# Performance work log

Hardware: AMD Instinct MI355X
Metric: run time of the kernel (lower is better)

The kernel has to match this reference:

```python
import jax, jax.numpy as jnp
import numpy as np

N_NODES = 100000
N_EDGES = 1600000
D_IN = 128
D_HID = 128
D_OUT = 128


def sage_conv(x, src, dst, W_l, b_l, W_r, n_nodes):
    # PyG SAGEConv (mean aggr): out = Linear_l(mean_j x_j) + Linear_r(x_i)
    msg = x[src]                                            # [E, d] gather
    agg = jax.ops.segment_sum(msg, dst, num_segments=n_nodes)  # [N, d]
    cnt = jax.ops.segment_sum(jnp.ones((src.shape[0],), x.dtype), dst,
                              num_segments=n_nodes)
    mean = agg / jnp.maximum(cnt, 1.0)[:, None]             # mean over neighbors
    return mean @ W_l.T + b_l + x @ W_r.T


def setup_inputs() -> dict:
    key = jax.random.key(0)
    ks = jax.random.split(key, 8)
    x = jax.random.normal(ks[0], (N_NODES, D_IN), dtype=jnp.float32)
    edge_index = jax.random.randint(ks[1], (2, N_EDGES), 0, N_NODES, dtype=jnp.int64)
    s1 = 1.0 / np.sqrt(D_IN)
    s2 = 1.0 / np.sqrt(D_HID)
    W1_l = jax.random.uniform(ks[2], (D_HID, D_IN), jnp.float32, -s1, s1)
    b1_l = jax.random.uniform(ks[3], (D_HID,), jnp.float32, -s1, s1)
    W1_r = jax.random.uniform(ks[4], (D_HID, D_IN), jnp.float32, -s1, s1)
    W2_l = jax.random.uniform(ks[5], (D_OUT, D_HID), jnp.float32, -s2, s2)
    b2_l = jax.random.uniform(ks[6], (D_OUT,), jnp.float32, -s2, s2)
    W2_r = jax.random.uniform(ks[7], (D_OUT, D_HID), jnp.float32, -s2, s2)
    return {"x": x, "edge_index": edge_index, "W1_l": W1_l, "b1_l": b1_l,
            "W1_r": W1_r, "W2_l": W2_l, "b2_l": b2_l, "W2_r": W2_r}


def reference(x, edge_index, W1_l, b1_l, W1_r, W2_l, b2_l, W2_r):
    src, dst = edge_index[0], edge_index[1]
    n = x.shape[0]
    h = sage_conv(x, src, dst, W1_l, b1_l, W1_r, n)
    h = jax.nn.relu(h)
    # F.dropout with training=False (eval mode) is identity
    out = sage_conv(h, src, dst, W2_l, b2_l, W2_r, n)
    return out
```

## Files before the change

### kernel.cpp

```cpp
#include <hip/hip_runtime.h>

typedef __attribute__((ext_vector_type(8))) short short8;
typedef __attribute__((ext_vector_type(4))) float f32x4;

#define NBMAX 512
#define CAP 8192

__device__ inline unsigned short f2bf(float f) {
  union { float f; unsigned u; } v; v.f = f;
  unsigned r = v.u + 0x7fffu + ((v.u >> 16) & 1u);
  return (unsigned short)(r >> 16);
}
__device__ inline float bf2f(unsigned short b) {
  union { unsigned u; float f; } v; v.u = ((unsigned)b) << 16;
  return v.f;
}

__device__ inline void addv8(float (&a)[8], uint4 v) {
  a[0] += bf2f((unsigned short)(v.x & 0xffffu));
  a[1] += bf2f((unsigned short)(v.x >> 16));
  a[2] += bf2f((unsigned short)(v.y & 0xffffu));
  a[3] += bf2f((unsigned short)(v.y >> 16));
  a[4] += bf2f((unsigned short)(v.z & 0xffffu));
  a[5] += bf2f((unsigned short)(v.z >> 16));
  a[6] += bf2f((unsigned short)(v.w & 0xffffu));
  a[7] += bf2f((unsigned short)(v.w >> 16));
}

__device__ inline int load_src(const int* ei, int E, int e, int f64) {
  return f64 ? ei[2 * e] : ei[e];
}
__device__ inline int load_dst(const int* ei, int E, int e, int f64) {
  return f64 ? ei[2 * (E + e)] : ei[E + e];
}

__global__ __launch_bounds__(256) void castbf(
    const float* __restrict__ x, unsigned short* __restrict__ xb, int n8,
    const float* __restrict__ W1l, const float* __restrict__ W1r,
    const float* __restrict__ W2l, const float* __restrict__ W2r,
    unsigned short* __restrict__ Wp) {
  const int nxb = gridDim.x - 4;
  const int b = blockIdx.x;
  const int tid = threadIdx.x;
  if (b >= nxb) {
    const int m = b - nxb;
    const float* W = (m == 0) ? W1l : (m == 1) ? W1r : (m == 2) ? W2l : W2r;
    unsigned short* dst = Wp + (size_t)m * 16384;
#pragma unroll
    for (int it = 0; it < 8; ++it) {
      int id = it * 256 + tid;
      int j = id >> 4;
      int kc = id & 15;
      int s = kc >> 2, q = kc & 3;
      int jt = j >> 4, nn2 = j & 15;
      int c = (s * 8 + jt) * 4 + q;
      const float* src = W + j * 128 + kc * 8;
      union { unsigned short u[8]; uint4 v; } t;
#pragma unroll
      for (int k = 0; k < 8; ++k) t.u[k] = f2bf(src[k]);
      *(uint4*)(dst + (c * 16 + nn2) * 8) = t.v;
    }
    return;
  }
  int i = b * 256 + tid;
  const int stride = nxb * 256;
  for (; i < n8; i += stride) {
    float4 v0 = ((const float4*)x)[2 * i];
    float4 v1 = ((const float4*)x)[2 * i + 1];
    union { unsigned short u[8]; uint4 v; } t;
    t.u[0] = f2bf(v0.x); t.u[1] = f2bf(v0.y);
    t.u[2] = f2bf(v0.z); t.u[3] = f2bf(v0.w);
    t.u[4] = f2bf(v1.x); t.u[5] = f2bf(v1.y);
    t.u[6] = f2bf(v1.z); t.u[7] = f2bf(v1.w);
    ((uint4*)xb)[i] = t.v;
  }
}

__global__ __launch_bounds__(256) void scatter2(
    const int* __restrict__ ei, int E,
    int* __restrict__ btot, int2* __restrict__ stage) {
  __shared__ int lcnt[NBMAX];
  __shared__ int lbase[NBMAX];
  __shared__ int sflag;
  const int t = threadIdx.x;
  if (t == 0) sflag = 0;
  for (int i = t; i < NBMAX; i += 256) lcnt[i] = 0;
  __syncthreads();
  const int e0 = blockIdx.x * 4096;
  {
    int e = e0 + t;
    int v = (e < E) ? ei[2 * e + 1] : 0;
    if (v) atomicOr(&sflag, 1);
  }
  __syncthreads();
  const int f64 = (sflag == 0) ? 1 : 0;

  int srcs[16], bks[16];
  int dsts[16];
#pragma unroll
  for (int i = 0; i < 16; ++i) {
    int e = e0 + i * 256 + t;
    if (e < E) {
      srcs[i] = load_src(ei, E, e, f64);
      int d = load_dst(ei, E, e, f64);
      dsts[i] = d;
      bks[i] = d >> 8;
      atomicAdd(&lcnt[d >> 8], 1);
    } else {
      bks[i] = -1;
    }
  }
  __syncthreads();
  for (int i = t; i < NBMAX; i += 256) {
    int c = lcnt[i];
    lbase[i] = c ? atomicAdd(&btot[i], c) : 0;
  }
  __syncthreads();
  for (int i = t; i < NBMAX; i += 256) lcnt[i] = 0;
  __syncthreads();
#pragma unroll
  for (int i = 0; i < 16; ++i) {
    int b = bks[i];
    if (b >= 0) {
      int r = atomicAdd(&lcnt[b], 1);
      stage[(size_t)b * CAP + lbase[b] + r] = make_int2(srcs[i], dsts[i]);
    }
  }
}

__global__ __launch_bounds__(256) void bucket_fill2(
    const int2* __restrict__ stage, const int* __restrict__ btot,
    int* __restrict__ offs, int* __restrict__ cnt, float* __restrict__ inv,
    int* __restrict__ csr, int N) {
  __shared__ int lhist[256];
  __shared__ int lscan[256];
  __shared__ int lcur[256];
  __shared__ int red[256];
  const int b = blockIdx.x;
  const int t = threadIdx.x;
  int sum = 0;
  for (int j = t; j < b; j += 256) sum += btot[j];
  red[t] = sum;
  lhist[t] = 0;
  __syncthreads();
  for (int d = 128; d; d >>= 1) {
    if (t < d) red[t] += red[t + d];
    __syncthreads();
  }
  const int base = red[0];
  const int count = btot[b];
  const int2* sp = stage + (size_t)b * CAP;
  for (int i = t; i < count; i += 256)
    atomicAdd(&lhist[sp[i].y & 255], 1);
  __syncthreads();
  int v = lhist[t];
  lscan[t] = v;
  __syncthreads();
  for (int d = 1; d < 256; d <<= 1) {
    int tv = (t >= d) ? lscan[t - d] : 0;
    __syncthreads();
    lscan[t] += tv;
    __syncthreads();
  }
  const int excl = lscan[t] - v;
  const int node = b * 256 + t;
  if (node < N) {
    offs[node] = base + excl;
    cnt[node] = v;
    inv[node] = 1.0f / (float)((v > 1) ? v : 1);
  }
  lcur[t] = base + excl;
  __syncthreads();
  for (int i = t; i < count; i += 256) {
    int2 sd = sp[i];
    int p = atomicAdd(&lcur[sd.y & 255], 1);
    csr[p] = sd.x;
  }
}

__global__ __launch_bounds__(256, 4) void agg_mean(
    const unsigned short* __restrict__ A, const float* __restrict__ inv,
    const int* __restrict__ offs, const int* __restrict__ cnt,
    const int* __restrict__ csr, unsigned short* __restrict__ M, int n) {
  int pr = (int)((blockIdx.x * 256 + threadIdx.x) >> 6);
  int n0 = pr * 2;
  if (n0 >= n) return;
  const int n1 = n0 + 1;
  const bool has1 = (n1 < n);
  const int lane = threadIdx.x & 63;
  const int g = lane >> 4;
  const int l = lane & 15;
  const int deg0 = cnt[n0];
  const int deg1 = has1 ? cnt[n1] : 0;
  const int start = offs[n0];
  const int T = deg0 + deg1;
  float acc0[8] = {0.f, 0.f, 0.f, 0.f, 0.f, 0.f, 0.f, 0.f};
  float acc1[8] = {0.f, 0.f, 0.f, 0.f, 0.f, 0.f, 0.f, 0.f};

  if (T <= 64) {
    int idx = (lane < T) ? csr[start + lane] : 0;
    int jmax = (T + 3) >> 2;
#pragma unroll 8
    for (int j = 0; j < jmax; ++j) {
      int e = j * 4 + g;
      int nbv = __shfl(idx, e);
      if (e < T) {
        uint4 v = *(const uint4*)(A + (size_t)nbv * 128 + l * 8);
        if (e < deg0) addv8(acc0, v);
        else addv8(acc1, v);
      }
    }
  } else {
    for (int node = 0; node < 2; ++node) {
      int dg = node ? deg1 : deg0;
      int st = node ? (start + deg0) : start;
      for (int base = 0; base < dg; base += 64) {
        int m = dg - base;
        if (m > 64) m = 64;
        int idx = (lane < m) ? csr[st + base + lane] : 0;
#pragma unroll 4
        for (int i = 0; i < m; i += 4) {
          int sl = i + g;
          int nbv = __shfl(idx, sl & 63);
          if (sl < m) {
            uint4 v = *(const uint4*)(A + (size_t)nbv * 128 + l * 8);
            if (node) addv8(acc1, v);
            else addv8(acc0, v);
          }
        }
      }
    }
  }

#pragma unroll
  for (int j = 0; j < 8; ++j) {
    acc0[j] += __shfl_xor(acc0[j], 16);
    acc0[j] += __shfl_xor(acc0[j], 32);
    acc1[j] += __shfl_xor(acc1[j], 16);
    acc1[j] += __shfl_xor(acc1[j], 32);
  }

  const int c0 = l * 8 + g * 2;
  {
    float s = inv[n0];
    unsigned pkt = (unsigned)f2bf(acc0[g * 2 + 0] * s) |
                   ((unsigned)f2bf(acc0[g * 2 + 1] * s) << 16);
    *(unsigned*)(M + (size_t)n0 * 128 + c0) = pkt;
  }
  if (has1) {
    float s = inv[n1];
    unsigned pkt = (unsigned)f2bf(acc1[g * 2 + 0] * s) |
                   ((unsigned)f2bf(acc1[g * 2 + 1] * s) << 16);
    *(unsigned*)(M + (size_t)n1 * 128 + c0) = pkt;
  }
}

template <int RELU, int OUTBF>
__global__ __launch_bounds__(256) void gemm_fused(
    const unsigned short* __restrict__ Am,
    const unsigned short* __restrict__ As,
    const unsigned short* __restrict__ Wp,
    const float* __restrict__ bias, void* __restrict__ outp, int n) {
  __shared__ unsigned short wsh[2 * 16384];
  const int tid = threadIdx.x;

  {
    const uint4* wsrc = (const uint4*)Wp;
    uint4* wdst = (uint4*)wsh;
#pragma unroll
    for (int it = 0; it < 16; ++it) {
      int id = it * 256 + tid;
      wdst[id] = wsrc[id];
    }
  }
  __syncthreads();

  const int lane = tid & 63;
  const int wave = tid >> 6;
  const int nn = lane & 15;
  const int quad = lane >> 4;
  const int rowbase = blockIdx.x * 64 + wave * 16;

  int nodeA = rowbase + nn;
  if (nodeA > n - 1) nodeA = n - 1;

  short8 am[4], asf[4];
#pragma unroll
  for (int s = 0; s < 4; ++s) {
    am[s] = *(const short8*)(Am + (size_t)nodeA * 128 + s * 32 + quad * 8);
    asf[s] = *(const short8*)(As + (size_t)nodeA * 128 + s * 32 + quad * 8);
  }

  f32x4 acc[8];
#pragma unroll
  for (int jt = 0; jt < 8; ++jt) acc[jt] = (f32x4){0.f, 0.f, 0.f, 0.f};

#pragma unroll
  for (int jt = 0; jt < 8; ++jt) {
#pragma unroll
    for (int s = 0; s < 4; ++s) {
      int c = (s * 8 + jt) * 4 + quad;
      short8 bl = *(const short8*)(wsh + (c * 16 + nn) * 8);
      short8 br = *(const short8*)(wsh + 16384 + (c * 16 + nn) * 8);
      acc[jt] = __builtin_amdgcn_mfma_f32_16x16x32_bf16(am[s], bl, acc[jt], 0, 0, 0);
      acc[jt] = __builtin_amdgcn_mfma_f32_16x16x32_bf16(asf[s], br, acc[jt], 0, 0, 0);
    }
  }

#pragma unroll
  for (int jt = 0; jt < 8; ++jt) {
    int col = jt * 16 + nn;
    float bv = bias[col];
#pragma unroll
    for (int r = 0; r < 4; ++r) {
      int ro = rowbase + quad * 4 + r;
      if (ro < n) {
        float o = acc[jt][r] + bv;
        if (RELU) o = fmaxf(o, 0.f);
        if (OUTBF) {
          ((unsigned short*)outp)[(size_t)ro * 128 + col] = f2bf(o);
        } else {
          ((float*)outp)[(size_t)ro * 128 + col] = o;
        }
      }
    }
  }
}


extern "C" void kernel_launch(void* const* d_in, const int* in_sizes, int n_in,
                              void* d_out, int out_size, void* d_ws, size_t ws_size,
                              hipStream_t stream) {
  const float* x = (const float*)d_in[0];
  const int* ei = (const int*)d_in[1];
  const float* W1l = (const float*)d_in[2];
  const float* b1 = (const float*)d_in[3];
  const float* W1r = (const float*)d_in[4];
  const float* W2l = (const float*)d_in[5];
  const float* b2 = (const float*)d_in[6];
  const float* W2r = (const float*)d_in[7];
  float* out = (float*)d_out;

  const int N = in_sizes[0] / 128;
  const int E = in_sizes[1] / 2;
  const int nb = (N + 255) / 256;

  char* p = (char*)d_ws;
  auto alloc = [&](size_t bytes) {
    char* r = p;
    p += (bytes + 255) & ~(size_t)255;
    return r;
  };
  int* btot = (int*)alloc((size_t)NBMAX * 4);
  int* cnt = (int*)alloc((size_t)N * 4);
  int* offs = (int*)alloc((size_t)N * 4);
  float* inv = (float*)alloc((size_t)N * 4);
  int* csr = (int*)alloc((size_t)E * 4);
  unsigned short* Mb = (unsigned short*)alloc((size_t)N * 128 * 2);
  unsigned short* Wpb = (unsigned short*)alloc((size_t)4 * 16384 * 2);
  size_t stage_bytes = (size_t)nb * CAP * 8;
  size_t hb_bytes = (size_t)N * 128 * 2;
  char* shared_region = alloc(stage_bytes > hb_bytes ? stage_bytes : hb_bytes);
  unsigned short* hb = (unsigned short*)shared_region;
  int2* stage = (int2*)shared_region;

  unsigned short* xb = (unsigned short*)d_out;

  hipMemsetAsync(btot, 0, (size_t)nb * 4, stream);

  castbf<<<2052, 256, 0, stream>>>(x, xb, N * 128 / 8, W1l, W1r, W2l, W2r, Wpb);
  scatter2<<<(E + 4095) / 4096, 256, 0, stream>>>(ei, E, btot, stage);
  bucket_fill2<<<nb, 256, 0, stream>>>(stage, btot, offs, cnt, inv, csr, N);

  const int gb = (N + 63) / 64;
  const int pairs = (N + 1) / 2;
  const int ab2 = (pairs + 3) / 4;

  agg_mean<<<ab2, 256, 0, stream>>>(xb, inv, offs, cnt, csr, Mb, N);
  gemm_fused<1, 1><<<gb, 256, 0, stream>>>(Mb, xb, Wpb, b1, (void*)hb, N);
  agg_mean<<<ab2, 256, 0, stream>>>(hb, inv, offs, cnt, csr, Mb, N);
  gemm_fused<0, 0><<<gb, 256, 0, stream>>>(Mb, hb, Wpb + 32768, b2, (void*)out, N);
}
```

Before: 344.3 us.

## Merge edge scatter with bf16 casts and batch neighbor loads in aggregation

Folds the edge-bucketing scatter kernel into the cast kernel so the x/weight conversions and scatter share one launch, with blocks split by index range. In agg_mean, the small-degree path now issues eight gathered row loads at once before accumulating, which raises memory-level parallelism. It also precomputes byte offsets (index<<8) and accumulates bf16 pairs into float2 vectors to cut unpack ALU work. This adds register pressure and loads padded lanes unconditionally (index 0 rows) when the degree is small.

```diff
diff --git a/kernel.cpp b/kernel.cpp
--- a/kernel.cpp
+++ b/kernel.cpp
@@ -2,6 +2,7 @@
 
 typedef __attribute__((ext_vector_type(8))) short short8;
 typedef __attribute__((ext_vector_type(4))) float f32x4;
+typedef __attribute__((ext_vector_type(2))) float f32x2;
 
 #define NBMAX 512
 #define CAP 8192
@@ -11,20 +12,13 @@
   unsigned r = v.u + 0x7fffu + ((v.u >> 16) & 1u);
   return (unsigned short)(r >> 16);
 }
-__device__ inline float bf2f(unsigned short b) {
-  union { unsigned u; float f; } v; v.u = ((unsigned)b) << 16;
-  return v.f;
-}
-
-__device__ inline void addv8(float (&a)[8], uint4 v) {
-  a[0] += bf2f((unsigned short)(v.x & 0xffffu));
-  a[1] += bf2f((unsigned short)(v.x >> 16));
-  a[2] += bf2f((unsigned short)(v.y & 0xffffu));
-  a[3] += bf2f((unsigned short)(v.y >> 16));
-  a[4] += bf2f((unsigned short)(v.z & 0xffffu));
-  a[5] += bf2f((unsigned short)(v.z >> 16));
-  a[6] += bf2f((unsigned short)(v.w & 0xffffu));
-  a[7] += bf2f((unsigned short)(v.w >> 16));
+
+__device__ inline void addf2(f32x2 (&a)[4], uint4 v) {
+  union { uint2 u; f32x2 f; } t;
+  t.u.x = v.x << 16; t.u.y = v.x & 0xffff0000u; a[0] += t.f;
+  t.u.x = v.y << 16; t.u.y = v.y & 0xffff0000u; a[1] += t.f;
+  t.u.x = v.z << 16; t.u.y = v.z & 0xffff0000u; a[2] += t.f;
+  t.u.x = v.w << 16; t.u.y = v.w & 0xffff0000u; a[3] += t.f;
 }
 
 __device__ inline int load_src(const int* ei, int E, int e, int f64) {
@@ -34,97 +28,100 @@
   return f64 ? ei[2 * (E + e)] : ei[E + e];
 }
 
-__global__ __launch_bounds__(256) void castbf(
+__global__ __launch_bounds__(256) void prep(
+    const int* __restrict__ ei, int E,
+    int* __restrict__ btot, int2* __restrict__ stage, int SB,
     const float* __restrict__ x, unsigned short* __restrict__ xb, int n8,
     const float* __restrict__ W1l, const float* __restrict__ W1r,
     const float* __restrict__ W2l, const float* __restrict__ W2r,
     unsigned short* __restrict__ Wp) {
-  const int nxb = gridDim.x - 4;
+  __shared__ int lcnt[NBMAX];
+  __shared__ int lbase[NBMAX];
+  __shared__ int sflag;
   const int b = blockIdx.x;
-  const int tid = threadIdx.x;
-  if (b >= nxb) {
-    const int m = b - nxb;
+  const int t = threadIdx.x;
+
+  if (b < SB) {
+    if (t == 0) sflag = 0;
+    for (int i = t; i < NBMAX; i += 256) lcnt[i] = 0;
+    __syncthreads();
+    const int e0 = b * 4096;
+    {
+      int e = e0 + t;
+      int v = (e < E) ? ei[2 * e + 1] : 0;
+      if (v) atomicOr(&sflag, 1);
+    }
+    __syncthreads();
+    const int f64 = (sflag == 0) ? 1 : 0;
+
+    int srcs[16], bks[16];
+    int dsts[16];
+#pragma unroll
+    for (int i = 0; i < 16; ++i) {
+      int e = e0 + i * 256 + t;
+      if (e < E) {
+        srcs[i] = load_src(ei, E, e, f64);
+        int d = load_dst(ei, E, e, f64);
+        dsts[i] = d;
+        bks[i] = d >> 8;
+        atomicAdd(&lcnt[d >> 8], 1);
+      } else {
+        bks[i] = -1;
+      }
+    }
+    __syncthreads();
+    for (int i = t; i < NBMAX; i += 256) {
+      int c = lcnt[i];
+      lbase[i] = c ? atomicAdd(&btot[i], c) : 0;
+    }
+    __syncthreads();
+    for (int i = t; i < NBMAX; i += 256) lcnt[i] = 0;
+    __syncthreads();
+#pragma unroll
+    for (int i = 0; i < 16; ++i) {
+      int bk = bks[i];
+      if (bk >= 0) {
+        int r = atomicAdd(&lcnt[bk], 1);
+        stage[(size_t)bk * CAP + lbase[bk] + r] = make_int2(srcs[i], dsts[i]);
+      }
+    }
+    return;
+  }
+
+  if (b < SB + 4) {
+    const int m = b - SB;
     const float* W = (m == 0) ? W1l : (m == 1) ? W1r : (m == 2) ? W2l : W2r;
     unsigned short* dst = Wp + (size_t)m * 16384;
 #pragma unroll
     for (int it = 0; it < 8; ++it) {
-      int id = it * 256 + tid;
+      int id = it * 256 + t;
       int j = id >> 4;
       int kc = id & 15;
       int s = kc >> 2, q = kc & 3;
       int jt = j >> 4, nn2 = j & 15;
       int c = (s * 8 + jt) * 4 + q;
       const float* src = W + j * 128 + kc * 8;
-      union { unsigned short u[8]; uint4 v; } t;
-#pragma unroll
-      for (int k = 0; k < 8; ++k) t.u[k] = f2bf(src[k]);
-      *(uint4*)(dst + (c * 16 + nn2) * 8) = t.v;
+      union { unsigned short u[8]; uint4 v; } tv;
+#pragma unroll
+      for (int k = 0; k < 8; ++k) tv.u[k] = f2bf(src[k]);
+      *(uint4*)(dst + (c * 16 + nn2) * 8) = tv.v;
     }
     return;
   }
-  int i = b * 256 + tid;
+
+  const int cb = b - SB - 4;
+  const int nxb = gridDim.x - SB - 4;
+  int i = cb * 256 + t;
   const int stride = nxb * 256;
   for (; i < n8; i += stride) {
     float4 v0 = ((const float4*)x)[2 * i];
     float4 v1 = ((const float4*)x)[2 * i + 1];
-    union { unsigned short u[8]; uint4 v; } t;
-    t.u[0] = f2bf(v0.x); t.u[1] = f2bf(v0.y);
-    t.u[2] = f2bf(v0.z); t.u[3] = f2bf(v0.w);
-    t.u[4] = f2bf(v1.x); t.u[5] = f2bf(v1.y);
-    t.u[6] = f2bf(v1.z); t.u[7] = f2bf(v1.w);
-    ((uint4*)xb)[i] = t.v;
-  }
-}
-
-__global__ __launch_bounds__(256) void scatter2(
-    const int* __restrict__ ei, int E,
-    int* __restrict__ btot, int2* __restrict__ stage) {
-  __shared__ int lcnt[NBMAX];
-  __shared__ int lbase[NBMAX];
-  __shared__ int sflag;
-  const int t = threadIdx.x;
-  if (t == 0) sflag = 0;
-  for (int i = t; i < NBMAX; i += 256) lcnt[i] = 0;
-  __syncthreads();
-  const int e0 = blockIdx.x * 4096;
-  {
-    int e = e0 + t;
-    int v = (e < E) ? ei[2 * e + 1] : 0;
-    if (v) atomicOr(&sflag, 1);
-  }
-  __syncthreads();
-  const int f64 = (sflag == 0) ? 1 : 0;
-
-  int srcs[16], bks[16];
-  int dsts[16];
-#pragma unroll
-  for (int i = 0; i < 16; ++i) {
-    int e = e0 + i * 256 + t;
-    if (e < E) {
-      srcs[i] = load_src(ei, E, e, f64);
-      int d = load_dst(ei, E, e, f64);
-      dsts[i] = d;
-      bks[i] = d >> 8;
-      atomicAdd(&lcnt[d >> 8], 1);
-    } else {
-      bks[i] = -1;
-    }
-  }
-  __syncthreads();
-  for (int i = t; i < NBMAX; i += 256) {
-    int c = lcnt[i];
-    lbase[i] = c ? atomicAdd(&btot[i], c) : 0;
-  }
-  __syncthreads();
-  for (int i = t; i < NBMAX; i += 256) lcnt[i] = 0;
-  __syncthreads();
-#pragma unroll
-  for (int i = 0; i < 16; ++i) {
-    int b = bks[i];
-    if (b >= 0) {
-      int r = atomicAdd(&lcnt[b], 1);
-      stage[(size_t)b * CAP + lbase[b] + r] = make_int2(srcs[i], dsts[i]);
-    }
+    union { unsigned short u[8]; uint4 v; } tv;
+    tv.u[0] = f2bf(v0.x); tv.u[1] = f2bf(v0.y);
+    tv.u[2] = f2bf(v0.z); tv.u[3] = f2bf(v0.w);
+    tv.u[4] = f2bf(v1.x); tv.u[5] = f2bf(v1.y);
+    tv.u[6] = f2bf(v1.z); tv.u[7] = f2bf(v1.w);
+    ((uint4*)xb)[i] = tv.v;
   }
 }
 
@@ -194,20 +191,40 @@
   const int deg1 = has1 ? cnt[n1] : 0;
   const int start = offs[n0];
   const int T = deg0 + deg1;
-  float acc0[8] = {0.f, 0.f, 0.f, 0.f, 0.f, 0.f, 0.f, 0.f};
-  float acc1[8] = {0.f, 0.f, 0.f, 0.f, 0.f, 0.f, 0.f, 0.f};
+  f32x2 acc0[4] = {{0.f, 0.f}, {0.f, 0.f}, {0.f, 0.f}, {0.f, 0.f}};
+  f32x2 acc1[4] = {{0.f, 0.f}, {0.f, 0.f}, {0.f, 0.f}, {0.f, 0.f}};
+  const char* Ab = (const char*)A + (size_t)l * 16;
 
   if (T <= 64) {
-    int idx = (lane < T) ? csr[start + lane] : 0;
-    int jmax = (T + 3) >> 2;
-#pragma unroll 8
-    for (int j = 0; j < jmax; ++j) {
-      int e = j * 4 + g;
-      int nbv = __shfl(idx, e);
-      if (e < T) {
-        uint4 v = *(const uint4*)(A + (size_t)nbv * 128 + l * 8);
-        if (e < deg0) addv8(acc0, v);
-        else addv8(acc1, v);
+    int offb = ((lane < T) ? csr[start + lane] : 0) << 8;
+    {
+      int nb[8];
+      uint4 vv[8];
+#pragma unroll
+      for (int j = 0; j < 8; ++j) nb[j] = __shfl(offb, j * 4 + g);
+#pragma unroll
+      for (int j = 0; j < 8; ++j)
+        vv[j] = *(const uint4*)(Ab + (size_t)(unsigned)nb[j]);
+#pragma unroll
+      for (int j = 0; j < 8; ++j) {
+        int e = j * 4 + g;
+        if (e < deg0) addf2(acc0, vv[j]);
+        else if (e < T) addf2(acc1, vv[j]);
+      }
+    }
+    if (T > 32) {
+      int nb[8];
+      uint4 vv[8];
+#pragma unroll
+      for (int j = 0; j < 8; ++j) nb[j] = __shfl(offb, 32 + j * 4 + g);
+#pragma unroll
+      for (int j = 0; j < 8; ++j)
+        vv[j] = *(const uint4*)(Ab + (size_t)(unsigned)nb[j]);
+#pragma unroll
+      for (int j = 0; j < 8; ++j) {
+        int e = 32 + j * 4 + g;
+        if (e < deg0) addf2(acc0, vv[j]);
+        else if (e < T) addf2(acc1, vv[j]);
       }
     }
   } else {
@@ -217,15 +234,15 @@
       for (int base = 0; base < dg; base += 64) {
         int m = dg - base;
         if (m > 64) m = 64;
-        int idx = (lane < m) ? csr[st + base + lane] : 0;
+        int offb = ((lane < m) ? csr[st + base + lane] : 0) << 8;
 #pragma unroll 4
         for (int i = 0; i < m; i += 4) {
           int sl = i + g;
-          int nbv = __shfl(idx, sl & 63);
+          int nbv = __shfl(offb, sl & 63);
           if (sl < m) {
-            uint4 v = *(const uint4*)(A + (size_t)nbv * 128 + l * 8);
-            if (node) addv8(acc1, v);
-            else addv8(acc0, v);
+            uint4 v = *(const uint4*)(Ab + (size_t)(unsigned)nbv);
+            if (node) addf2(acc1, v);
+            else addf2(acc0, v);
           }
         }
       }
@@ -233,24 +250,28 @@
   }
 
 #pragma unroll
-  for (int j = 0; j < 8; ++j) {
-    acc0[j] += __shfl_xor(acc0[j], 16);
-    acc0[j] += __shfl_xor(acc0[j], 32);
-    acc1[j] += __shfl_xor(acc1[j], 16);
-    acc1[j] += __shfl_xor(acc1[j], 32);
+  for (int k = 0; k < 4; ++k) {
+    acc0[k].x += __shfl_xor(acc0[k].x, 16);
+    acc0[k].x += __shfl_xor(acc0[k].x, 32);
+    acc0[k].y += __shfl_xor(acc0[k].y, 16);
+    acc0[k].y += __shfl_xor(acc0[k].y, 32);
+    acc1[k].x += __shfl_xor(acc1[k].x, 16);
+    acc1[k].x += __shfl_xor(acc1[k].x, 32);
+    acc1[k].y += __shfl_xor(acc1[k].y, 16);
+    acc1[k].y += __shfl_xor(acc1[k].y, 32);
   }
 
   const int c0 = l * 8 + g * 2;
   {
     float s = inv[n0];
-    unsigned pkt = (unsigned)f2bf(acc0[g * 2 + 0] * s) |
-                   ((unsigned)f2bf(acc0[g * 2 + 1] * s) << 16);
+    unsigned pkt = (unsigned)f2bf(acc0[g].x * s) |
+                   ((unsigned)f2bf(acc0[g].y * s) << 16);
     *(unsigned*)(M + (size_t)n0 * 128 + c0) = pkt;
   }
   if (has1) {
     float s = inv[n1];
-    unsigned pkt = (unsigned)f2bf(acc1[g * 2 + 0] * s) |
-                   ((unsigned)f2bf(acc1[g * 2 + 1] * s) << 16);
+    unsigned pkt = (unsigned)f2bf(acc1[g].x * s) |
+                   ((unsigned)f2bf(acc1[g].y * s) << 16);
     *(unsigned*)(M + (size_t)n1 * 128 + c0) = pkt;
   }
 }
@@ -368,8 +389,10 @@
 
   hipMemsetAsync(btot, 0, (size_t)nb * 4, stream);
 
-  castbf<<<2052, 256, 0, stream>>>(x, xb, N * 128 / 8, W1l, W1r, W2l, W2r, Wpb);
-  scatter2<<<(E + 4095) / 4096, 256, 0, stream>>>(ei, E, btot, stage);
+  const int SB = (E + 4095) / 4096;
+  prep<<<SB + 4 + 2048, 256, 0, stream>>>(ei, E, btot, stage, SB,
+                                          x, xb, N * 128 / 8,
+                                          W1l, W1r, W2l, W2r, Wpb);
   bucket_fill2<<<nb, 256, 0, stream>>>(stage, btot, offs, cnt, inv, csr, N);
 
   const int gb = (N + 63) / 64;
```

New measurement: 323.7 us. -6.0%, faster.
